# Kernel optimization log

Measured on AMD Instinct MI355X. Metric: run time of the kernel, lower is better.

The kernel has to match this reference:

```python
import jax, jax.numpy as jnp
import numpy as np

FP8_MAX = 448.0  # float8_e4m3 max finite value


def setup_inputs() -> dict:
    key = jax.random.key(0)
    k1, k2, k3, k4, k5 = jax.random.split(key, 5)
    B, S, IN, OUT = 8, 2048, 2048, 2048
    x = jax.random.normal(k1, (B, S, IN), dtype=jnp.float32)
    weight = jax.random.normal(k2, (OUT, IN), dtype=jnp.float32) * 0.02
    bias = jax.random.normal(k3, (OUT,), dtype=jnp.float32)
    # per-tensor scales, kept positive and away from zero
    scale_in = jax.random.uniform(k4, (1,), dtype=jnp.float32) * 0.09 + 0.01
    scale_w = jax.random.uniform(k5, (1,), dtype=jnp.float32) * 0.09 + 0.01
    return {"x": x, "weight": weight, "bias": bias,
            "scale_in": scale_in, "scale_w": scale_w}


def _fp8_quantize(x, scale):
    # divide by scale, saturate to fp8 range, cast to fp8 e4m3
    q = jnp.clip(x / scale, -FP8_MAX, FP8_MAX)
    return q.astype(jnp.float8_e4m3fn)


def reference(x, weight, bias, scale_in, scale_w):
    # quantize input and weight to fp8 (per-tensor scales)
    xq = _fp8_quantize(x, scale_in)            # [B,S,IN] fp8
    wq = _fp8_quantize(weight, scale_w)        # [OUT,IN] fp8
    # scaled matmul: accumulate in fp32, dequant with scale_a*scale_b, emit fp16
    acc = jnp.einsum('bsk,nk->bsn', xq.astype(jnp.float32), wq.astype(jnp.float32))
    out = (acc * (scale_in[0] * scale_w[0])).astype(jnp.float16)
    out = out + bias.astype(jnp.float16)       # trailing bias add at fp16
    return out
```

## Files before the change

### kernel.cpp

```cpp
#include <hip/hip_runtime.h>
#include <hip/hip_fp16.h>
#include <stdint.h>

#define MDIM 16384
#define NDIM 2048
#define KDIM 2048

typedef __attribute__((ext_vector_type(4))) float f32x4;
typedef __attribute__((ext_vector_type(4))) int   i32x4;
typedef __attribute__((ext_vector_type(8))) int   i32x8;

__device__ __forceinline__ unsigned f32_to_e4m3(float x) {
    float q = fminf(448.f, fmaxf(-448.f, x));
    unsigned ub = __float_as_uint(q);
    unsigned sgn = (ub >> 24) & 0x80u;
    float aq = fabsf(q);
    int E = (int)((__float_as_uint(aq) >> 23) & 0xff) - 127;
    if (E < -6) E = -6;
    float quantum = __uint_as_float((unsigned)(E + 124) << 23);
    int m = (int)rintf(aq / quantum);
    if (m == 16) { m = 8; E += 1; }
    unsigned bits;
    if (m < 8) bits = sgn | (unsigned)m;
    else       bits = sgn | ((unsigned)(E + 7) << 3) | (unsigned)(m - 8);
    return bits;
}

__global__ void quant_fp8_kernel(const float* __restrict__ x,
                                 uint8_t* __restrict__ q,
                                 const float* __restrict__ scale,
                                 unsigned n16) {
    float sc = scale[0];
    unsigned i = blockIdx.x * blockDim.x + threadIdx.x;
    unsigned stride = gridDim.x * blockDim.x;
    for (; i < n16; i += stride) {
        const float4* xp = (const float4*)(x + (size_t)i * 16);
        uint32_t w[4];
#pragma unroll
        for (int j = 0; j < 4; ++j) {
            float4 v = xp[j];
            unsigned b0 = f32_to_e4m3(v.x / sc);
            unsigned b1 = f32_to_e4m3(v.y / sc);
            unsigned b2 = f32_to_e4m3(v.z / sc);
            unsigned b3 = f32_to_e4m3(v.w / sc);
            w[j] = b0 | (b1 << 8) | (b2 << 16) | (b3 << 24);
        }
        ((uint4*)q)[i] = make_uint4(w[0], w[1], w[2], w[3]);
    }
}

#define BM 256
#define BN 256
#define BKB 128
#define NKT (KDIM / BKB)

__device__ __forceinline__ void gload_lds16(const uint8_t* g, uint8_t* l) {
    __builtin_amdgcn_global_load_lds(
        (const __attribute__((address_space(1))) void*)g,
        (__attribute__((address_space(3))) void*)l, 16, 0, 0);
}

__device__ __forceinline__ void barrier_fenced() {
    asm volatile("" ::: "memory");
    __builtin_amdgcn_s_barrier();
    asm volatile("" ::: "memory");
}

__global__ __launch_bounds__(512) void gemm_fp8_kernel(
    const uint8_t* __restrict__ Aq, const uint8_t* __restrict__ Bq,
    const float* __restrict__ bias, const float* __restrict__ s_in,
    const float* __restrict__ s_w, float* __restrict__ out) {

    extern __shared__ uint8_t lds[];

    int nwg = gridDim.x;
    int cpx = nwg >> 3;
    int bid = blockIdx.x;
    int swz = (bid & 7) * cpx + (bid >> 3);
    int tm = swz >> 3;
    int tn = swz & 7;
    int row0 = tm * BM;
    int col0 = tn * BN;

    int tid  = threadIdx.x;
    int lane = tid & 63;
    int wid  = tid >> 6;
    int wr = wid >> 2, wc = wid & 3;
    int r15 = lane & 15;
    int g   = lane >> 4;

    int perm0 = ((2 * g + r15) & 7) << 4;
    int perm1 = ((2 * g + 1 + r15) & 7) << 4;

    int pj[2]   = {tid, 512 + tid};
    int rj[2], cj[2];
#pragma unroll
    for (int j = 0; j < 2; ++j) {
        rj[j] = pj[j] >> 3;
        cj[j] = ((pj[j] & 7) - (rj[j] & 7)) & 7;
    }
    size_t asrcoff[2], bsrcoff[2];
    int    adst[2], bdst[2];
#pragma unroll
    for (int j = 0; j < 2; ++j) {
        int ar = (rj[j] & 63) + ((rj[j] >> 6) << 7);
        asrcoff[j] = (size_t)ar * KDIM + cj[j] * 16;
        bsrcoff[j] = (size_t)rj[j] * KDIM + cj[j] * 16;
        adst[j] = pj[j] * 16;
        bdst[j] = 32768 + pj[j] * 16;
    }

    const uint8_t* Asrc = Aq + (size_t)row0 * KDIM;
    const uint8_t* Bsrc = Bq + (size_t)col0 * KDIM;
    uint8_t* stdst = &lds[0];

#define STAGE_A(U, KT)                                                        \
    {                                                                         \
        _Pragma("unroll")                                                     \
        for (int j_ = 0; j_ < 2; ++j_)                                        \
            gload_lds16(Asrc + asrcoff[j_] + (size_t)(U) * 64 * KDIM +        \
                            (size_t)(KT) * BKB,                               \
                        stdst + adst[j_] + (U) * 16384);                      \
    }
#define STAGE_B(U, KT)                                                        \
    {                                                                         \
        _Pragma("unroll")                                                     \
        for (int j_ = 0; j_ < 2; ++j_)                                        \
            gload_lds16(Bsrc + bsrcoff[j_] + (size_t)(U) * 128 * KDIM +       \
                            (size_t)(KT) * BKB,                               \
                        stdst + bdst[j_] + (U) * 16384);                      \
    }

    f32x4 acc[8][4];
#pragma unroll
    for (int m = 0; m < 8; ++m)
#pragma unroll
        for (int n = 0; n < 4; ++n)
            acc[m][n] = (f32x4){0.f, 0.f, 0.f, 0.f};

    STAGE_A(0, 0); STAGE_B(0, 0); STAGE_B(1, 0); STAGE_A(1, 0);
    asm volatile("s_waitcnt vmcnt(2)" ::: "memory");
    barrier_fenced();

    int aRowBase = wr * 64;
    int bUnit = (wc >> 1) * 1024;
    int bRowBase = (wc & 1) * 64;

    i32x8 bf[4], af[4];

#define LOAD_BF(bo)                                                           \
    _Pragma("unroll")                                                         \
    for (int n_ = 0; n_ < 4; ++n_) {                                          \
        int rB = bRowBase + n_ * 16 + r15;                                    \
        const uint8_t* rp = lds + (bo) + 32768 + (bUnit + rB * 8) * 16;       \
        i32x4 lo = *(const i32x4*)(rp + perm0);                               \
        i32x4 hi = *(const i32x4*)(rp + perm1);                               \
        _Pragma("unroll")                                                     \
        for (int q_ = 0; q_ < 4; ++q_) { bf[n_][q_] = lo[q_]; bf[n_][4 + q_] = hi[q_]; } \
    }

#define LOAD_AF(bo, MH)                                                       \
    _Pragma("unroll")                                                         \
    for (int m_ = 0; m_ < 4; ++m_) {                                          \
        int rA = aRowBase + m_ * 16 + r15;                                    \
        const uint8_t* rp = lds + (bo) + ((MH) * 1024 + rA * 8) * 16;         \
        i32x4 lo = *(const i32x4*)(rp + perm0);                               \
        i32x4 hi = *(const i32x4*)(rp + perm1);                               \
        _Pragma("unroll")                                                     \
        for (int q_ = 0; q_ < 4; ++q_) { af[m_][q_] = lo[q_]; af[m_][4 + q_] = hi[q_]; } \
    }

#define MFMA_BLOCK(MH)                                                        \
    __builtin_amdgcn_s_setprio(1);                                            \
    _Pragma("unroll")                                                         \
    for (int m_ = 0; m_ < 4; ++m_)                                            \
        _Pragma("unroll")                                                     \
        for (int n_ = 0; n_ < 4; ++n_)                                        \
            acc[(MH) * 4 + m_][n_] =                                          \
                __builtin_amdgcn_mfma_scale_f32_16x16x128_f8f6f4(             \
                    af[m_], bf[n_], acc[(MH) * 4 + m_][n_],                   \
                    0, 0, 0, 127, 0, 127);                                    \
    __builtin_amdgcn_s_setprio(0);

    for (int t = 0; t < NKT; ++t) {
        const unsigned bo = (unsigned)(t & 1) << 16;
        stdst = &lds[(unsigned)((t + 1) & 1) << 16];
        if (t + 1 < NKT) {
            STAGE_A(0, t + 1);
            STAGE_B(0, t + 1);
            LOAD_BF(bo);
            LOAD_AF(bo, 0);
            MFMA_BLOCK(0);
            asm volatile("s_waitcnt vmcnt(4)" ::: "memory");
            barrier_fenced();
            STAGE_B(1, t + 1);
            STAGE_A(1, t + 1);
            LOAD_AF(bo, 1);
            MFMA_BLOCK(1);
            asm volatile("s_waitcnt vmcnt(2)" ::: "memory");
            barrier_fenced();
        } else {
            LOAD_BF(bo);
            LOAD_AF(bo, 0);
            MFMA_BLOCK(0);
            asm volatile("s_waitcnt vmcnt(0)" ::: "memory");
            barrier_fenced();
            LOAD_AF(bo, 1);
            MFMA_BLOCK(1);
        }
    }

    float s = s_in[0] * s_w[0];
    int g4 = g * 4;
#pragma unroll
    for (int n = 0; n < 4; ++n) {
        int col = col0 + wc * 64 + n * 16 + r15;
        __half hb = __float2half(bias[col]);
#pragma unroll
        for (int mh = 0; mh < 2; ++mh)
#pragma unroll
            for (int m = 0; m < 4; ++m) {
                int rbase = row0 + wr * 128 + mh * 64 + m * 16 + g4;
#pragma unroll
                for (int r = 0; r < 4; ++r) {
                    __half h = __float2half(acc[mh * 4 + m][n][r] * s);
                    out[(size_t)(rbase + r) * NDIM + col] =
                        __half2float(__hadd(h, hb));
                }
            }
    }
#undef STAGE_A
#undef STAGE_B
#undef LOAD_BF
#undef LOAD_AF
#undef MFMA_BLOCK
}

extern "C" void kernel_launch(void* const* d_in, const int* in_sizes, int n_in,
                              void* d_out, int out_size, void* d_ws, size_t ws_size,
                              hipStream_t stream) {
    const float* x      = (const float*)d_in[0];
    const float* weight = (const float*)d_in[1];
    const float* bias   = (const float*)d_in[2];
    const float* s_in   = (const float*)d_in[3];
    const float* s_w    = (const float*)d_in[4];
    float* out          = (float*)d_out;

    uint8_t* xq = (uint8_t*)d_ws;
    uint8_t* wq = (uint8_t*)d_ws + (size_t)MDIM * KDIM;

    quant_fp8_kernel<<<2048, 256, 0, stream>>>(x, xq, s_in,
        (unsigned)((size_t)MDIM * KDIM / 16));
    quant_fp8_kernel<<<512, 256, 0, stream>>>(weight, wq, s_w,
        (unsigned)((size_t)NDIM * KDIM / 16));

    dim3 grid((MDIM / BM) * (NDIM / BN));
    gemm_fp8_kernel<<<grid, 512, 131072, stream>>>(xq, wq, bias, s_in, s_w, out);
}
```

Baseline: 129.7 us.

## Deepen GEMM prefetch, merge quant kernels, use reciprocal multiply in fp8 rounding

The GEMM main loop is reorganised so the second half of tile t+1 and the first half of tile t+2 are staged into LDS while the current tile is being computed. This gives a deeper cross-iteration prefetch, and the vmcnt waits and barriers are rearranged to match. The two quantization launches are merged into one kernel that splits its blocks between x and the weight, saving a launch. The fp8 rounding now multiplies by a power-of-two reciprocal instead of dividing. The reworked buffer reuse and wait counts risk a race if the counts are wrong.

```diff
diff --git a/kernel.cpp b/kernel.cpp
--- a/kernel.cpp
+++ b/kernel.cpp
@@ -17,8 +17,8 @@
     float aq = fabsf(q);
     int E = (int)((__float_as_uint(aq) >> 23) & 0xff) - 127;
     if (E < -6) E = -6;
-    float quantum = __uint_as_float((unsigned)(E + 124) << 23);
-    int m = (int)rintf(aq / quantum);
+    float rq = __uint_as_float((unsigned)(130 - E) << 23);
+    int m = (int)rintf(aq * rq);
     if (m == 16) { m = 8; E += 1; }
     unsigned bits;
     if (m < 8) bits = sgn | (unsigned)m;
@@ -26,14 +26,11 @@
     return bits;
 }
 
-__global__ void quant_fp8_kernel(const float* __restrict__ x,
-                                 uint8_t* __restrict__ q,
-                                 const float* __restrict__ scale,
-                                 unsigned n16) {
-    float sc = scale[0];
-    unsigned i = blockIdx.x * blockDim.x + threadIdx.x;
-    unsigned stride = gridDim.x * blockDim.x;
-    for (; i < n16; i += stride) {
+__device__ __forceinline__ void quant_span(const float* __restrict__ x,
+                                           uint8_t* __restrict__ q, float sc,
+                                           unsigned i0, unsigned stride,
+                                           unsigned n16) {
+    for (unsigned i = i0; i < n16; i += stride) {
         const float4* xp = (const float4*)(x + (size_t)i * 16);
         uint32_t w[4];
 #pragma unroll
@@ -49,6 +46,23 @@
     }
 }
 
+__global__ void quant_both_kernel(const float* __restrict__ x,
+                                  uint8_t* __restrict__ xq,
+                                  const float* __restrict__ w,
+                                  uint8_t* __restrict__ wq,
+                                  const float* __restrict__ s_in,
+                                  const float* __restrict__ s_w) {
+    if (blockIdx.x < 2048) {
+        unsigned i0 = blockIdx.x * blockDim.x + threadIdx.x;
+        quant_span(x, xq, s_in[0], i0, 2048 * 256,
+                   (unsigned)((size_t)MDIM * KDIM / 16));
+    } else {
+        unsigned i0 = (blockIdx.x - 2048) * blockDim.x + threadIdx.x;
+        quant_span(w, wq, s_w[0], i0, 256 * 256,
+                   (unsigned)((size_t)NDIM * KDIM / 16));
+    }
+}
+
 #define BM 256
 #define BN 256
 #define BKB 128
@@ -92,7 +106,7 @@
     int perm0 = ((2 * g + r15) & 7) << 4;
     int perm1 = ((2 * g + 1 + r15) & 7) << 4;
 
-    int pj[2]   = {tid, 512 + tid};
+    int pj[2] = {tid, 512 + tid};
     int rj[2], cj[2];
 #pragma unroll
     for (int j = 0; j < 2; ++j) {
@@ -112,23 +126,22 @@
 
     const uint8_t* Asrc = Aq + (size_t)row0 * KDIM;
     const uint8_t* Bsrc = Bq + (size_t)col0 * KDIM;
-    uint8_t* stdst = &lds[0];
-
-#define STAGE_A(U, KT)                                                        \
+
+#define STAGE_A(U, KT, DST)                                                   \
     {                                                                         \
         _Pragma("unroll")                                                     \
         for (int j_ = 0; j_ < 2; ++j_)                                        \
             gload_lds16(Asrc + asrcoff[j_] + (size_t)(U) * 64 * KDIM +        \
                             (size_t)(KT) * BKB,                               \
-                        stdst + adst[j_] + (U) * 16384);                      \
-    }
-#define STAGE_B(U, KT)                                                        \
+                        (DST) + adst[j_] + (U) * 16384);                      \
+    }
+#define STAGE_B(U, KT, DST)                                                   \
     {                                                                         \
         _Pragma("unroll")                                                     \
         for (int j_ = 0; j_ < 2; ++j_)                                        \
             gload_lds16(Bsrc + bsrcoff[j_] + (size_t)(U) * 128 * KDIM +       \
                             (size_t)(KT) * BKB,                               \
-                        stdst + bdst[j_] + (U) * 16384);                      \
+                        (DST) + bdst[j_] + (U) * 16384);                      \
     }
 
     f32x4 acc[8][4];
@@ -138,9 +151,14 @@
         for (int n = 0; n < 4; ++n)
             acc[m][n] = (f32x4){0.f, 0.f, 0.f, 0.f};
 
-    STAGE_A(0, 0); STAGE_B(0, 0); STAGE_B(1, 0); STAGE_A(1, 0);
-    asm volatile("s_waitcnt vmcnt(2)" ::: "memory");
-    barrier_fenced();
+    {
+        uint8_t* b0 = &lds[0];
+        uint8_t* b1 = &lds[65536];
+        STAGE_A(0, 0, b0); STAGE_B(0, 0, b0); STAGE_B(1, 0, b0); STAGE_A(1, 0, b0);
+        STAGE_A(0, 1, b1); STAGE_B(0, 1, b1);
+        asm volatile("s_waitcnt vmcnt(4)" ::: "memory");
+        barrier_fenced();
+    }
 
     int aRowBase = wr * 64;
     int bUnit = (wc >> 1) * 1024;
@@ -184,30 +202,19 @@
 
     for (int t = 0; t < NKT; ++t) {
         const unsigned bo = (unsigned)(t & 1) << 16;
-        stdst = &lds[(unsigned)((t + 1) & 1) << 16];
-        if (t + 1 < NKT) {
-            STAGE_A(0, t + 1);
-            STAGE_B(0, t + 1);
-            LOAD_BF(bo);
-            LOAD_AF(bo, 0);
-            MFMA_BLOCK(0);
-            asm volatile("s_waitcnt vmcnt(4)" ::: "memory");
-            barrier_fenced();
-            STAGE_B(1, t + 1);
-            STAGE_A(1, t + 1);
-            LOAD_AF(bo, 1);
-            MFMA_BLOCK(1);
-            asm volatile("s_waitcnt vmcnt(2)" ::: "memory");
-            barrier_fenced();
-        } else {
-            LOAD_BF(bo);
-            LOAD_AF(bo, 0);
-            MFMA_BLOCK(0);
-            asm volatile("s_waitcnt vmcnt(0)" ::: "memory");
-            barrier_fenced();
-            LOAD_AF(bo, 1);
-            MFMA_BLOCK(1);
-        }
+        uint8_t* nbuf = &lds[(unsigned)((t + 1) & 1) << 16];
+        uint8_t* cbuf = &lds[bo];
+        if (t + 1 < NKT) { STAGE_B(1, t + 1, nbuf); STAGE_A(1, t + 1, nbuf); }
+        LOAD_BF(bo);
+        LOAD_AF(bo, 0);
+        MFMA_BLOCK(0);
+        barrier_fenced();
+        if (t + 2 < NKT) { STAGE_A(0, t + 2, cbuf); STAGE_B(0, t + 2, cbuf); }
+        LOAD_AF(bo, 1);
+        MFMA_BLOCK(1);
+        if (t + 2 < NKT)      asm volatile("s_waitcnt vmcnt(4)" ::: "memory");
+        else if (t + 1 < NKT) asm volatile("s_waitcnt vmcnt(0)" ::: "memory");
+        barrier_fenced();
     }
 
     float s = s_in[0] * s_w[0];
@@ -249,10 +256,7 @@
     uint8_t* xq = (uint8_t*)d_ws;
     uint8_t* wq = (uint8_t*)d_ws + (size_t)MDIM * KDIM;
 
-    quant_fp8_kernel<<<2048, 256, 0, stream>>>(x, xq, s_in,
-        (unsigned)((size_t)MDIM * KDIM / 16));
-    quant_fp8_kernel<<<512, 256, 0, stream>>>(weight, wq, s_w,
-        (unsigned)((size_t)NDIM * KDIM / 16));
+    quant_both_kernel<<<2304, 256, 0, stream>>>(x, xq, weight, wq, s_in, s_w);
 
     dim3 grid((MDIM / BM) * (NDIM / BN));
     gemm_fp8_kernel<<<grid, 512, 131072, stream>>>(xq, wq, bias, s_in, s_w, out);
```

After: 119.6 us. 1.08x faster.
